# Kernel tuning notes

Measured on AMD Instinct MI355X. Metric: run time of the kernel, lower is better.

## Reference

```python
import jax, jax.numpy as jnp
import numpy as np

USER_NUM = 100000
ITEM_NUM = 50000
EMBED_DIM = 64
N_LAYERS = 2
NNZ_UU, NNZ_UI, NNZ_II = 1600000, 2000000, 800000


def setup_inputs() -> dict:
    key = jax.random.key(0)
    ks = jax.random.split(key, 11)
    return {
        "user_embedding": jax.random.normal(ks[0], (USER_NUM, EMBED_DIM), jnp.float32),
        "item_embedding": jax.random.normal(ks[1], (ITEM_NUM, EMBED_DIM), jnp.float32),
        "uu_val": jax.random.uniform(ks[2], (NNZ_UU,), jnp.float32),
        "ui_val": jax.random.uniform(ks[3], (NNZ_UI,), jnp.float32),
        "ii_val": jax.random.uniform(ks[4], (NNZ_II,), jnp.float32),
        "uu_rows": jax.random.randint(ks[5], (NNZ_UU,), 0, USER_NUM, jnp.int32),
        "uu_cols": jax.random.randint(ks[6], (NNZ_UU,), 0, USER_NUM, jnp.int32),
        "ui_rows": jax.random.randint(ks[7], (NNZ_UI,), 0, USER_NUM, jnp.int32),
        "ui_cols": jax.random.randint(ks[8], (NNZ_UI,), 0, ITEM_NUM, jnp.int32),
        "ii_rows": jax.random.randint(ks[9], (NNZ_II,), 0, ITEM_NUM, jnp.int32),
        "ii_cols": jax.random.randint(ks[10], (NNZ_II,), 0, ITEM_NUM, jnp.int32),
    }


def _spmm(rows, cols, vals, x, n_out):
    # sparse(COO) @ dense: gather source features, scale by edge value, scatter-add to rows
    return jax.ops.segment_sum(vals[:, None] * x[cols], rows, num_segments=n_out)


def reference(user_embedding, item_embedding, uu_val, ui_val, ii_val,
              uu_rows, uu_cols, ui_rows, ui_cols, ii_rows, ii_cols):
    u = user_embedding
    i = item_embedding
    # running sum for mean over (n_layers + 1) layer outputs
    u_sum, i_sum = u, i
    for _ in range(N_LAYERS):
        u_from_i = _spmm(ui_rows, ui_cols, ui_val, i, USER_NUM)        # user_item_graph @ item
        i_from_u = _spmm(ui_cols, ui_rows, ui_val, u, ITEM_NUM)        # user_item_graph.T @ user
        uu = _spmm(uu_rows, uu_cols, uu_val, u, USER_NUM)              # user_graph @ user
        ii = _spmm(ii_rows, ii_cols, ii_val, i, ITEM_NUM)              # item_graph @ item
        u = 0.5 * (uu + u_from_i)   # mean over stacked pair
        i = 0.5 * (ii + i_from_u)
        u_sum = u_sum + u
        i_sum = i_sum + i
    inv = 1.0 / (N_LAYERS + 1)
    return u_sum * inv, i_sum * inv
```

## Files before the change

### kernel.cpp

```cpp
#include <hip/hip_runtime.h>

typedef _Float16 half8_t __attribute__((ext_vector_type(8)));
typedef _Float16 half4_t __attribute__((ext_vector_type(4)));

#define NU 100000
#define NI 50000
#define NR (NU + NI)
#define D 64
#define COARSE 1024
#define RPB 147
#define CAP 8800
#define CHUNK 6144
#define RPT 6
#define NT4 (NR * 16)

__global__ void init_kernel(const float4* __restrict__ ue, const float4* __restrict__ ie,
                            float4* __restrict__ out, half4_t* __restrict__ curh) {
    int idx = blockIdx.x * 256 + threadIdx.x;
    if (idx >= NT4) return;
    float4 v = (idx < NU * 16) ? ue[idx] : ie[idx - NU * 16];
    out[idx] = v;
    half4_t h;
    h[0] = (_Float16)v.x; h[1] = (_Float16)v.y; h[2] = (_Float16)v.z; h[3] = (_Float16)v.w;
    curh[idx] = h;
}

__device__ __forceinline__ int place_dest(int p, const int* ui_r, const int* ui_c,
                                          const int* uu_r, const int* ii_r,
                                          int n_ui, int n_uu) {
    if (p < 2 * n_ui) {
        int e = p >> 1;
        return (p & 1) ? NU + ui_c[e] : ui_r[e];
    } else if (p < 2 * n_ui + n_uu) {
        return uu_r[p - 2 * n_ui];
    } else {
        return NU + ii_r[p - 2 * n_ui - n_uu];
    }
}

__global__ void count_kernel(const int* __restrict__ ui_r, const int* __restrict__ ui_c,
                             const int* __restrict__ uu_r, const int* __restrict__ ii_r,
                             int* __restrict__ m, int n_ui, int n_uu, int nnzt) {
    __shared__ int cnt[COARSE];
    int tid = threadIdx.x;
    cnt[tid] = 0;
    __syncthreads();
    int blk0 = blockIdx.x * CHUNK;
#pragma unroll
    for (int k = 0; k < RPT; k++) {
        int p = blk0 + k * 1024 + tid;
        if (p < nnzt) {
            int dest = place_dest(p, ui_r, ui_c, uu_r, ii_r, n_ui, n_uu);
            atomicAdd(&cnt[dest / RPB], 1);
        }
    }
    __syncthreads();
    m[blockIdx.x * COARSE + tid] = cnt[tid];
}

__global__ void colsum_kernel(const int* __restrict__ m, int* __restrict__ tots, int nblk) {
    __shared__ int s[256];
    int c = blockIdx.x, tid = threadIdx.x;
    int sum = 0;
    for (int b = tid; b < nblk; b += 256) sum += m[b * COARSE + c];
    s[tid] = sum;
    __syncthreads();
    for (int off = 128; off > 0; off >>= 1) {
        if (tid < off) s[tid] += s[tid + off];
        __syncthreads();
    }
    if (tid == 0) tots[c] = s[0];
}

__global__ void scan1_kernel(const int* __restrict__ tots, int* __restrict__ coarse_base,
                             int* __restrict__ ptr_nr) {
    __shared__ int s[COARSE];
    int tid = threadIdx.x;
    int x = tots[tid];
    s[tid] = x;
    __syncthreads();
    for (int off = 1; off < COARSE; off <<= 1) {
        int t = (tid >= off) ? s[tid - off] : 0;
        __syncthreads();
        s[tid] += t;
        __syncthreads();
    }
    coarse_base[tid] = s[tid] - x;
    if (tid == COARSE - 1) {
        coarse_base[COARSE] = s[tid];
        *ptr_nr = s[tid];
    }
}

__global__ void rebase_kernel(int* __restrict__ m, const int* __restrict__ coarse_base, int nblk) {
    __shared__ int s[256];
    int c = blockIdx.x, tid = threadIdx.x;
    int K = (nblk + 255) / 256;
    int b0 = tid * K;
    int b1 = b0 + K;
    if (b1 > nblk) b1 = nblk;
    int sum = 0;
    for (int b = b0; b < b1; b++) sum += m[b * COARSE + c];
    s[tid] = sum;
    __syncthreads();
    for (int off = 1; off < 256; off <<= 1) {
        int t = (tid >= off) ? s[tid - off] : 0;
        __syncthreads();
        s[tid] += t;
        __syncthreads();
    }
    int run = coarse_base[c] + s[tid] - sum;
    for (int b = b0; b < b1; b++) {
        int v = m[b * COARSE + c];
        m[b * COARSE + c] = run;
        run += v;
    }
}

__global__ void place_kernel(const int* __restrict__ ui_r, const int* __restrict__ ui_c,
                             const float* __restrict__ ui_v,
                             const int* __restrict__ uu_r, const int* __restrict__ uu_c,
                             const float* __restrict__ uu_v,
                             const int* __restrict__ ii_r, const int* __restrict__ ii_c,
                             const float* __restrict__ ii_v,
                             const int* __restrict__ m, uint2* __restrict__ scratch,
                             int n_ui, int n_uu, int nnzt) {
    __shared__ uint2 rec[CHUNK];
    __shared__ int cnt[COARSE];
    __shared__ int lbase[COARSE];
    __shared__ int base_s[COARSE];
    __shared__ int s_ntot;
    int tid = threadIdx.x;
    cnt[tid] = 0;
    __syncthreads();
    int blk0 = blockIdx.x * CHUNK;
    int rk[RPT];
#pragma unroll
    for (int k = 0; k < RPT; k++) {
        int p = blk0 + k * 1024 + tid;
        rk[k] = -1;
        if (p < nnzt) {
            int dest = place_dest(p, ui_r, ui_c, uu_r, ii_r, n_ui, n_uu);
            int c = dest / RPB;
            int lr = atomicAdd(&cnt[c], 1);
            rk[k] = (c << 14) | lr;
        }
    }
    __syncthreads();
    int own = cnt[tid];
    lbase[tid] = own;
    __syncthreads();
    for (int off = 1; off < COARSE; off <<= 1) {
        int t = (tid >= off) ? lbase[tid - off] : 0;
        __syncthreads();
        lbase[tid] += t;
        __syncthreads();
    }
    int incl = lbase[tid];
    __syncthreads();
    lbase[tid] = incl - own;
    if (tid == COARSE - 1) s_ntot = incl;
    base_s[tid] = m[blockIdx.x * COARSE + tid];
    __syncthreads();
#pragma unroll
    for (int k = 0; k < RPT; k++) {
        int p = blk0 + k * 1024 + tid;
        if (p >= nnzt) continue;
        int dest, src;
        float v;
        if (p < 2 * n_ui) {
            int e = p >> 1;
            int r = ui_r[e], cc = ui_c[e];
            v = ui_v[e];
            if (p & 1) { dest = NU + cc; src = r; }
            else       { dest = r; src = NU + cc; }
        } else if (p < 2 * n_ui + n_uu) {
            int e = p - 2 * n_ui;
            dest = uu_r[e]; src = uu_c[e]; v = uu_v[e];
        } else {
            int e = p - 2 * n_ui - n_uu;
            dest = NU + ii_r[e]; src = NU + ii_c[e]; v = ii_v[e];
        }
        int c  = rk[k] >> 14;
        int lr = rk[k] & 0x3FFF;
        int dl = dest - c * RPB;
        _Float16 hv = (_Float16)v;
        unsigned short us;
        __builtin_memcpy(&us, &hv, 2);
        rec[lbase[c] + lr] = make_uint2(((unsigned)dl << 18) | (unsigned)src,
                                        ((unsigned)c << 16) | (unsigned)us);
    }
    __syncthreads();
    int ntot = s_ntot;
    for (int i = tid; i < ntot; i += 1024) {
        uint2 r = rec[i];
        int c = r.y >> 16;
        scratch[base_s[c] + (i - lbase[c])] = r;
    }
}

__global__ void csr_kernel(const uint2* __restrict__ scratch, const int* __restrict__ coarse_base,
                           int* __restrict__ ptr, int* __restrict__ pk_src,
                           unsigned short* __restrict__ pk_val) {
    __shared__ int s[1024];
    __shared__ int fine[256];
    __shared__ int fill[256];
    __shared__ int lsrc[CAP];
    __shared__ unsigned short lval[CAP];
    int c = blockIdx.x, tid = threadIdx.x;
    int rbeg = c * RPB;
    int rcnt = NR - rbeg;
    if (rcnt > RPB) rcnt = RPB;
    if (rcnt < 0) rcnt = 0;
    int base = coarse_base[c], end = coarse_base[c + 1];
    int n = end - base;
    if (tid < 256) fine[tid] = 0;
    __syncthreads();
    for (int i = tid; i < n; i += 1024)
        atomicAdd(&fine[scratch[base + i].x >> 18], 1);
    __syncthreads();
    int own = (tid < 256) ? fine[tid] : 0;
    s[tid] = own;
    __syncthreads();
    for (int off = 1; off < 256; off <<= 1) {
        int t = (tid >= off) ? s[tid - off] : 0;
        __syncthreads();
        s[tid] += t;
        __syncthreads();
    }
    int excl = s[tid] - own;
    if (tid < rcnt) ptr[rbeg + tid] = base + excl;
    if (tid < 256) fill[tid] = excl;
    __syncthreads();
    if (n <= CAP) {
        for (int i = tid; i < n; i += 1024) {
            uint2 rec = scratch[base + i];
            int dl = rec.x >> 18;
            int slot = atomicAdd(&fill[dl], 1);
            lsrc[slot] = rec.x & 0x3FFFF;
            lval[slot] = (unsigned short)rec.y;
        }
        __syncthreads();
        for (int i = tid; i < n; i += 1024) {
            pk_src[base + i] = lsrc[i] << 7;
            pk_val[base + i] = lval[i];
        }
    } else {
        for (int i = tid; i < n; i += 1024) {
            uint2 rec = scratch[base + i];
            int dl = rec.x >> 18;
            int slot = atomicAdd(&fill[dl], 1);
            pk_src[base + slot] = (rec.x & 0x3FFFF) << 7;
            pk_val[base + slot] = (unsigned short)rec.y;
        }
    }
}

__global__ void spmm_fused(const int* __restrict__ ptr, const int* __restrict__ pk_src,
                           const _Float16* __restrict__ pk_val,
                           const half8_t* __restrict__ src,
                           half8_t* __restrict__ nexth, float4* __restrict__ out,
                           float final_scale, int store_next) {
    int w = (int)((blockIdx.x * blockDim.x + threadIdx.x) >> 6);
    int lane = threadIdx.x & 63;
    if (w >= NR) return;
    int g = lane >> 3;
    int fl = lane & 7;
    const char* sp = (const char*)src;
    int flo = fl * 16;

    int b = ptr[w], e = ptr[w + 1];
    float acc[8];
#pragma unroll
    for (int k = 0; k < 8; k++) acc[k] = 0.f;

    for (int j = b; j < e; j += 32) {
#pragma unroll
        for (int t = 0; t < 4; t++) {
            int jt = j + 8 * t + g;
            int it = (jt < e) ? jt : b;
            int st = pk_src[it];
            float vt = (jt < e) ? (float)pk_val[it] : 0.f;
            half8_t xt = *(const half8_t*)(sp + st + flo);
#pragma unroll
            for (int k = 0; k < 8; k++) acc[k] += vt * (float)xt[k];
        }
    }

#pragma unroll
    for (int k = 0; k < 8; k++) {
        acc[k] += __shfl_xor(acc[k], 8);
        acc[k] += __shfl_xor(acc[k], 16);
        acc[k] += __shfl_xor(acc[k], 32);
    }

    if (lane < 8) {
        float h[8];
#pragma unroll
        for (int k = 0; k < 8; k++) h[k] = 0.5f * acc[k];
        if (store_next) {
            half8_t hh;
#pragma unroll
            for (int k = 0; k < 8; k++) hh[k] = (_Float16)h[k];
            nexth[w * 8 + lane] = hh;
        }
        float4* op = out + (size_t)w * 16 + lane * 2;
        float4 o0 = op[0];
        float4 o1 = op[1];
        o0.x = (o0.x + h[0]) * final_scale;
        o0.y = (o0.y + h[1]) * final_scale;
        o0.z = (o0.z + h[2]) * final_scale;
        o0.w = (o0.w + h[3]) * final_scale;
        o1.x = (o1.x + h[4]) * final_scale;
        o1.y = (o1.y + h[5]) * final_scale;
        o1.z = (o1.z + h[6]) * final_scale;
        o1.w = (o1.w + h[7]) * final_scale;
        op[0] = o0;
        op[1] = o1;
    }
}

extern "C" void kernel_launch(void* const* d_in, const int* in_sizes, int n_in,
                              void* d_out, int out_size, void* d_ws, size_t ws_size,
                              hipStream_t stream) {
    const float* ue      = (const float*)d_in[0];
    const float* ie      = (const float*)d_in[1];
    const float* uu_val  = (const float*)d_in[2];
    const float* ui_val  = (const float*)d_in[3];
    const float* ii_val  = (const float*)d_in[4];
    const int*   uu_rows = (const int*)d_in[5];
    const int*   uu_cols = (const int*)d_in[6];
    const int*   ui_rows = (const int*)d_in[7];
    const int*   ui_cols = (const int*)d_in[8];
    const int*   ii_rows = (const int*)d_in[9];
    const int*   ii_cols = (const int*)d_in[10];

    const int NNZ_UU = in_sizes[2];
    const int NNZ_UI = in_sizes[3];
    const int NNZ_II = in_sizes[4];
    const int NNZT   = 2 * NNZ_UI + NNZ_UU + NNZ_II;
    const int NBLK   = (NNZT + CHUNK - 1) / CHUNK;

    float* out = (float*)d_out;

    char* wsb = (char*)d_ws;
    half8_t* curh   = (half8_t*)wsb;
    uint2*   scratch = (uint2*)(wsb + (size_t)NR * 128);
    half8_t* nexth  = (half8_t*)scratch;
    int*     pk_src = (int*)(scratch + NNZT);
    unsigned short* pk_val = (unsigned short*)(pk_src + NNZT);
    int*     ptr    = (int*)(pk_val + NNZT);
    int*     coarse_base = ptr + (NR + 1);
    int*     tots   = coarse_base + (COARSE + 1);
    int*     m      = tots + COARSE;

    init_kernel<<<(NT4 + 255) / 256, 256, 0, stream>>>(
        (const float4*)ue, (const float4*)ie, (float4*)out, (half4_t*)curh);

    count_kernel<<<NBLK, 1024, 0, stream>>>(
        ui_rows, ui_cols, uu_rows, ii_rows, m, NNZ_UI, NNZ_UU, NNZT);

    colsum_kernel<<<COARSE, 256, 0, stream>>>(m, tots, NBLK);
    scan1_kernel<<<1, 1024, 0, stream>>>(tots, coarse_base, ptr + NR);
    rebase_kernel<<<COARSE, 256, 0, stream>>>(m, coarse_base, NBLK);

    place_kernel<<<NBLK, 1024, 0, stream>>>(
        ui_rows, ui_cols, ui_val, uu_rows, uu_cols, uu_val,
        ii_rows, ii_cols, ii_val, m, scratch, NNZ_UI, NNZ_UU, NNZT);

    csr_kernel<<<COARSE, 1024, 0, stream>>>(scratch, coarse_base, ptr, pk_src, pk_val);

    int blocks = (NR * 64 + 511) / 512;

    spmm_fused<<<blocks, 512, 0, stream>>>(
        ptr, pk_src, (const _Float16*)pk_val, curh, nexth, (float4*)out, 1.0f, 1);

    spmm_fused<<<blocks, 512, 0, stream>>>(
        ptr, pk_src, (const _Float16*)pk_val, nexth, curh, (float4*)out, 1.0f / 3.0f, 0);
}
```

Measured before the change: 515.4 us.

## Pad CSR rows to multiples of four for vectorized edge loads in SpMM

The CSR build now pads each row's edge list to a multiple of four, with zero-filled slots and per-coarse-block slack, so row pointers are 4-aligned. The SpMM kernel then reads source indices as int4 and values as half4, each lane group handling eight edges per iteration with eight independent gathers in flight. This is meant to cut the number of index/value load instructions and raise memory-level parallelism in the gather loop. In exchange the padded edge arrays are larger, padded slots still gather row 0 with zero weight, and csr_kernel does extra zeroing work.

```diff
diff --git a/kernel.cpp b/kernel.cpp
--- a/kernel.cpp
+++ b/kernel.cpp
@@ -13,6 +13,7 @@
 #define CHUNK 6144
 #define RPT 6
 #define NT4 (NR * 16)
+#define PKSLACK 448
 
 __global__ void init_kernel(const float4* __restrict__ ue, const float4* __restrict__ ie,
                             float4* __restrict__ out, half4_t* __restrict__ curh) {
@@ -207,6 +208,7 @@
     __shared__ int fill[256];
     __shared__ int lsrc[CAP];
     __shared__ unsigned short lval[CAP];
+    __shared__ int s_pn;
     int c = blockIdx.x, tid = threadIdx.x;
     int rbeg = c * RPB;
     int rcnt = NR - rbeg;
@@ -214,13 +216,16 @@
     if (rcnt < 0) rcnt = 0;
     int base = coarse_base[c], end = coarse_base[c + 1];
     int n = end - base;
+    int pkc    = ((base + 3) & ~3) + c * PKSLACK;
+    int pknext = ((end  + 3) & ~3) + (c + 1) * PKSLACK;
     if (tid < 256) fine[tid] = 0;
     __syncthreads();
     for (int i = tid; i < n; i += 1024)
         atomicAdd(&fine[scratch[base + i].x >> 18], 1);
     __syncthreads();
     int own = (tid < 256) ? fine[tid] : 0;
-    s[tid] = own;
+    int own4 = (own + 3) & ~3;
+    s[tid] = own4;
     __syncthreads();
     for (int off = 1; off < 256; off <<= 1) {
         int t = (tid >= off) ? s[tid - off] : 0;
@@ -228,11 +233,16 @@
         s[tid] += t;
         __syncthreads();
     }
-    int excl = s[tid] - own;
-    if (tid < rcnt) ptr[rbeg + tid] = base + excl;
-    if (tid < 256) fill[tid] = excl;
-    __syncthreads();
-    if (n <= CAP) {
+    int excl4 = s[tid] - own4;
+    if (tid < rcnt) ptr[rbeg + tid] = pkc + excl4;
+    if (tid == 0 && rbeg + rcnt == NR) ptr[NR] = pknext;
+    if (tid < 256) fill[tid] = excl4;
+    if (tid == 255) s_pn = s[255];
+    __syncthreads();
+    int pn = s_pn;
+    if (pn <= CAP) {
+        for (int i = tid; i < pn; i += 1024) { lsrc[i] = 0; lval[i] = 0; }
+        __syncthreads();
         for (int i = tid; i < n; i += 1024) {
             uint2 rec = scratch[base + i];
             int dl = rec.x >> 18;
@@ -241,23 +251,26 @@
             lval[slot] = (unsigned short)rec.y;
         }
         __syncthreads();
-        for (int i = tid; i < n; i += 1024) {
-            pk_src[base + i] = lsrc[i] << 7;
-            pk_val[base + i] = lval[i];
-        }
+        for (int i = tid; i < pn; i += 1024) {
+            pk_src[pkc + i] = lsrc[i] << 7;
+            pk_val[pkc + i] = lval[i];
+        }
+        for (int i = pkc + pn + tid; i < pknext; i += 1024) { pk_src[i] = 0; pk_val[i] = 0; }
     } else {
+        for (int i = pkc + tid; i < pknext; i += 1024) { pk_src[i] = 0; pk_val[i] = 0; }
+        __syncthreads();
         for (int i = tid; i < n; i += 1024) {
             uint2 rec = scratch[base + i];
             int dl = rec.x >> 18;
             int slot = atomicAdd(&fill[dl], 1);
-            pk_src[base + slot] = (rec.x & 0x3FFFF) << 7;
-            pk_val[base + slot] = (unsigned short)rec.y;
+            pk_src[pkc + slot] = (rec.x & 0x3FFFF) << 7;
+            pk_val[pkc + slot] = (unsigned short)rec.y;
         }
     }
 }
 
 __global__ void spmm_fused(const int* __restrict__ ptr, const int* __restrict__ pk_src,
-                           const _Float16* __restrict__ pk_val,
+                           const half4_t* __restrict__ pk_val4,
                            const half8_t* __restrict__ src,
                            half8_t* __restrict__ nexth, float4* __restrict__ out,
                            float final_scale, int store_next) {
@@ -266,24 +279,45 @@
     if (w >= NR) return;
     int g = lane >> 3;
     int fl = lane & 7;
-    const char* sp = (const char*)src;
-    int flo = fl * 16;
+    const char* sph = (const char*)src + (fl << 4);
+    const int4* ps = (const int4*)pk_src;
 
     int b = ptr[w], e = ptr[w + 1];
+    int q0 = b >> 2, qe = e >> 2;
+
     float acc[8];
 #pragma unroll
     for (int k = 0; k < 8; k++) acc[k] = 0.f;
 
-    for (int j = b; j < e; j += 32) {
-#pragma unroll
-        for (int t = 0; t < 4; t++) {
-            int jt = j + 8 * t + g;
-            int it = (jt < e) ? jt : b;
-            int st = pk_src[it];
-            float vt = (jt < e) ? (float)pk_val[it] : 0.f;
-            half8_t xt = *(const half8_t*)(sp + st + flo);
-#pragma unroll
-            for (int k = 0; k < 8; k++) acc[k] += vt * (float)xt[k];
+    for (int q = q0 + g; q < qe; q += 16) {
+        int qb = q + 8;
+        int4 sa = ps[q];
+        half4_t va = pk_val4[q];
+        int4 sb = ps[qb];
+        half4_t vb = pk_val4[qb];
+        if (qb >= qe) {
+            sb = make_int4(0, 0, 0, 0);
+            half4_t z = {};
+            vb = z;
+        }
+        half8_t x0 = *(const half8_t*)(sph + sa.x);
+        half8_t x1 = *(const half8_t*)(sph + sa.y);
+        half8_t x2 = *(const half8_t*)(sph + sa.z);
+        half8_t x3 = *(const half8_t*)(sph + sa.w);
+        half8_t x4 = *(const half8_t*)(sph + sb.x);
+        half8_t x5 = *(const half8_t*)(sph + sb.y);
+        half8_t x6 = *(const half8_t*)(sph + sb.z);
+        half8_t x7 = *(const half8_t*)(sph + sb.w);
+#pragma unroll
+        for (int k = 0; k < 8; k++) {
+            acc[k] += (float)va[0] * (float)x0[k];
+            acc[k] += (float)va[1] * (float)x1[k];
+            acc[k] += (float)va[2] * (float)x2[k];
+            acc[k] += (float)va[3] * (float)x3[k];
+            acc[k] += (float)vb[0] * (float)x4[k];
+            acc[k] += (float)vb[1] * (float)x5[k];
+            acc[k] += (float)vb[2] * (float)x6[k];
+            acc[k] += (float)vb[3] * (float)x7[k];
         }
     }
 
@@ -340,6 +374,7 @@
     const int NNZ_II = in_sizes[4];
     const int NNZT   = 2 * NNZ_UI + NNZ_UU + NNZ_II;
     const int NBLK   = (NNZT + CHUNK - 1) / CHUNK;
+    const int PKTOT  = NNZT + PKSLACK * COARSE + 64;
 
     float* out = (float*)d_out;
 
@@ -348,8 +383,8 @@
     uint2*   scratch = (uint2*)(wsb + (size_t)NR * 128);
     half8_t* nexth  = (half8_t*)scratch;
     int*     pk_src = (int*)(scratch + NNZT);
-    unsigned short* pk_val = (unsigned short*)(pk_src + NNZT);
-    int*     ptr    = (int*)(pk_val + NNZT);
+    unsigned short* pk_val = (unsigned short*)(pk_src + PKTOT);
+    int*     ptr    = (int*)(pk_val + PKTOT);
     int*     coarse_base = ptr + (NR + 1);
     int*     tots   = coarse_base + (COARSE + 1);
     int*     m      = tots + COARSE;
@@ -373,8 +408,8 @@
     int blocks = (NR * 64 + 511) / 512;
 
     spmm_fused<<<blocks, 512, 0, stream>>>(
-        ptr, pk_src, (const _Float16*)pk_val, curh, nexth, (float4*)out, 1.0f, 1);
+        ptr, pk_src, (const half4_t*)pk_val, curh, nexth, (float4*)out, 1.0f, 1);
 
     spmm_fused<<<blocks, 512, 0, stream>>>(
-        ptr, pk_src, (const _Float16*)pk_val, nexth, curh, (float4*)out, 1.0f / 3.0f, 0);
-}
+        ptr, pk_src, (const half4_t*)pk_val, nexth, curh, (float4*)out, 1.0f / 3.0f, 0);
+}
```

Result: slower. 556.7 us (+8.0%).

## Segment CSR by source-column range and process four rows per 8-lane group

Applied to the files above, without the earlier changes.

The CSR build now buckets edges by source segment (src>>14) and by 1024-row destination chunk. This produces ten per-segment row-pointer arrays, so during SpMM all gathers within a segment pass touch a limited slice of the source features, which should improve L2 locality. The SpMM kernel is rewritten so each 8-lane group owns four consecutive rows, looping over segments with 4-way unrolled edge processing instead of one wavefront per row. In exchange it adds ten pointer reads per row, serial per-row loops that can load-imbalance on long rows, and heavier scans in the preprocessing.

```diff
diff --git a/kernel.cpp b/kernel.cpp
--- a/kernel.cpp
+++ b/kernel.cpp
@@ -7,8 +7,10 @@
 #define NI 50000
 #define NR (NU + NI)
 #define D 64
-#define COARSE 1024
-#define RPB 147
+#define SEG 10
+#define SEGSH 14
+#define CHK 147
+#define COARSE (SEG * CHK)
 #define CAP 8800
 #define CHUNK 6144
 #define RPT 6
@@ -25,37 +27,45 @@
     curh[idx] = h;
 }
 
-__device__ __forceinline__ int place_dest(int p, const int* ui_r, const int* ui_c,
-                                          const int* uu_r, const int* ii_r,
-                                          int n_ui, int n_uu) {
+__device__ __forceinline__ void place_ds(int p, const int* ui_r, const int* ui_c,
+                                         const int* uu_r, const int* uu_c,
+                                         const int* ii_r, const int* ii_c,
+                                         int n_ui, int n_uu, int& dest, int& src) {
     if (p < 2 * n_ui) {
         int e = p >> 1;
-        return (p & 1) ? NU + ui_c[e] : ui_r[e];
+        int r = ui_r[e], c = ui_c[e];
+        if (p & 1) { dest = NU + c; src = r; }
+        else       { dest = r;      src = NU + c; }
     } else if (p < 2 * n_ui + n_uu) {
-        return uu_r[p - 2 * n_ui];
+        int e = p - 2 * n_ui;
+        dest = uu_r[e]; src = uu_c[e];
     } else {
-        return NU + ii_r[p - 2 * n_ui - n_uu];
+        int e = p - 2 * n_ui - n_uu;
+        dest = NU + ii_r[e]; src = NU + ii_c[e];
     }
 }
 
 __global__ void count_kernel(const int* __restrict__ ui_r, const int* __restrict__ ui_c,
-                             const int* __restrict__ uu_r, const int* __restrict__ ii_r,
+                             const int* __restrict__ uu_r, const int* __restrict__ uu_c,
+                             const int* __restrict__ ii_r, const int* __restrict__ ii_c,
                              int* __restrict__ m, int n_ui, int n_uu, int nnzt) {
     __shared__ int cnt[COARSE];
     int tid = threadIdx.x;
-    cnt[tid] = 0;
+    for (int i = tid; i < COARSE; i += 1024) cnt[i] = 0;
     __syncthreads();
     int blk0 = blockIdx.x * CHUNK;
 #pragma unroll
     for (int k = 0; k < RPT; k++) {
         int p = blk0 + k * 1024 + tid;
         if (p < nnzt) {
-            int dest = place_dest(p, ui_r, ui_c, uu_r, ii_r, n_ui, n_uu);
-            atomicAdd(&cnt[dest / RPB], 1);
-        }
-    }
-    __syncthreads();
-    m[blockIdx.x * COARSE + tid] = cnt[tid];
+            int dest, src;
+            place_ds(p, ui_r, ui_c, uu_r, uu_c, ii_r, ii_c, n_ui, n_uu, dest, src);
+            int key = (src >> SEGSH) * CHK + (dest >> 10);
+            atomicAdd(&cnt[key], 1);
+        }
+    }
+    __syncthreads();
+    for (int i = tid; i < COARSE; i += 1024) m[blockIdx.x * COARSE + i] = cnt[i];
 }
 
 __global__ void colsum_kernel(const int* __restrict__ m, int* __restrict__ tots, int nblk) {
@@ -72,24 +82,23 @@
     if (tid == 0) tots[c] = s[0];
 }
 
-__global__ void scan1_kernel(const int* __restrict__ tots, int* __restrict__ coarse_base,
-                             int* __restrict__ ptr_nr) {
-    __shared__ int s[COARSE];
+__global__ void scan1_kernel(const int* __restrict__ tots, int* __restrict__ coarse_base) {
+    __shared__ int s[2048];
     int tid = threadIdx.x;
-    int x = tots[tid];
-    s[tid] = x;
-    __syncthreads();
-    for (int off = 1; off < COARSE; off <<= 1) {
-        int t = (tid >= off) ? s[tid - off] : 0;
-        __syncthreads();
-        s[tid] += t;
-        __syncthreads();
-    }
-    coarse_base[tid] = s[tid] - x;
-    if (tid == COARSE - 1) {
-        coarse_base[COARSE] = s[tid];
-        *ptr_nr = s[tid];
-    }
+    int x0 = (tid < COARSE) ? tots[tid] : 0;
+    int x1 = (tid + 1024 < COARSE) ? tots[tid + 1024] : 0;
+    s[tid] = x0; s[tid + 1024] = x1;
+    __syncthreads();
+    for (int off = 1; off < 2048; off <<= 1) {
+        int a = (tid >= off) ? s[tid - off] : 0;
+        int b = (tid + 1024 >= off) ? s[tid + 1024 - off] : 0;
+        __syncthreads();
+        s[tid] += a; s[tid + 1024] += b;
+        __syncthreads();
+    }
+    if (tid < COARSE) coarse_base[tid] = s[tid] - x0;
+    if (tid + 1024 < COARSE) coarse_base[tid + 1024] = s[tid + 1024] - x1;
+    if (tid == 0) coarse_base[COARSE] = s[2047];
 }
 
 __global__ void rebase_kernel(int* __restrict__ m, const int* __restrict__ coarse_base, int nblk) {
@@ -126,12 +135,11 @@
                              const int* __restrict__ m, uint2* __restrict__ scratch,
                              int n_ui, int n_uu, int nnzt) {
     __shared__ uint2 rec[CHUNK];
-    __shared__ int cnt[COARSE];
-    __shared__ int lbase[COARSE];
+    __shared__ int cnt[2048];
+    __shared__ int lb[2048];
     __shared__ int base_s[COARSE];
-    __shared__ int s_ntot;
     int tid = threadIdx.x;
-    cnt[tid] = 0;
+    cnt[tid] = 0; cnt[tid + 1024] = 0;
     __syncthreads();
     int blk0 = blockIdx.x * CHUNK;
     int rk[RPT];
@@ -140,27 +148,25 @@
         int p = blk0 + k * 1024 + tid;
         rk[k] = -1;
         if (p < nnzt) {
-            int dest = place_dest(p, ui_r, ui_c, uu_r, ii_r, n_ui, n_uu);
-            int c = dest / RPB;
-            int lr = atomicAdd(&cnt[c], 1);
-            rk[k] = (c << 14) | lr;
-        }
-    }
-    __syncthreads();
-    int own = cnt[tid];
-    lbase[tid] = own;
-    __syncthreads();
-    for (int off = 1; off < COARSE; off <<= 1) {
-        int t = (tid >= off) ? lbase[tid - off] : 0;
-        __syncthreads();
-        lbase[tid] += t;
-        __syncthreads();
-    }
-    int incl = lbase[tid];
-    __syncthreads();
-    lbase[tid] = incl - own;
-    if (tid == COARSE - 1) s_ntot = incl;
-    base_s[tid] = m[blockIdx.x * COARSE + tid];
+            int dest, src;
+            place_ds(p, ui_r, ui_c, uu_r, uu_c, ii_r, ii_c, n_ui, n_uu, dest, src);
+            int key = (src >> SEGSH) * CHK + (dest >> 10);
+            int lr = atomicAdd(&cnt[key], 1);
+            rk[k] = (key << 14) | lr;
+        }
+    }
+    __syncthreads();
+    int o0 = cnt[tid], o1 = cnt[tid + 1024];
+    lb[tid] = o0; lb[tid + 1024] = o1;
+    __syncthreads();
+    for (int off = 1; off < 2048; off <<= 1) {
+        int a = (tid >= off) ? lb[tid - off] : 0;
+        int b = (tid + 1024 >= off) ? lb[tid + 1024 - off] : 0;
+        __syncthreads();
+        lb[tid] += a; lb[tid + 1024] += b;
+        __syncthreads();
+    }
+    for (int i = tid; i < COARSE; i += 1024) base_s[i] = m[blockIdx.x * COARSE + i];
     __syncthreads();
 #pragma unroll
     for (int k = 0; k < RPT; k++) {
@@ -183,62 +189,64 @@
         }
         int c  = rk[k] >> 14;
         int lr = rk[k] & 0x3FFF;
-        int dl = dest - c * RPB;
+        int dl = dest & 1023;
         _Float16 hv = (_Float16)v;
         unsigned short us;
         __builtin_memcpy(&us, &hv, 2);
-        rec[lbase[c] + lr] = make_uint2(((unsigned)dl << 18) | (unsigned)src,
-                                        ((unsigned)c << 16) | (unsigned)us);
-    }
-    __syncthreads();
-    int ntot = s_ntot;
+        rec[(lb[c] - cnt[c]) + lr] = make_uint2(((unsigned)dl << 18) | (unsigned)src,
+                                                ((unsigned)c << 16) | (unsigned)us);
+    }
+    __syncthreads();
+    int ntot = lb[2047];
     for (int i = tid; i < ntot; i += 1024) {
         uint2 r = rec[i];
         int c = r.y >> 16;
-        scratch[base_s[c] + (i - lbase[c])] = r;
+        scratch[base_s[c] + (i - (lb[c] - cnt[c]))] = r;
     }
 }
 
 __global__ void csr_kernel(const uint2* __restrict__ scratch, const int* __restrict__ coarse_base,
-                           int* __restrict__ ptr, int* __restrict__ pk_src,
+                           int* __restrict__ P, int* __restrict__ pk_src,
                            unsigned short* __restrict__ pk_val) {
     __shared__ int s[1024];
-    __shared__ int fine[256];
-    __shared__ int fill[256];
+    __shared__ int fine[1024];
+    __shared__ int fill[1024];
     __shared__ int lsrc[CAP];
     __shared__ unsigned short lval[CAP];
     int c = blockIdx.x, tid = threadIdx.x;
-    int rbeg = c * RPB;
+    int seg = c / CHK, chunk = c % CHK;
+    int rbeg = chunk << 10;
     int rcnt = NR - rbeg;
-    if (rcnt > RPB) rcnt = RPB;
+    if (rcnt > 1024) rcnt = 1024;
     if (rcnt < 0) rcnt = 0;
     int base = coarse_base[c], end = coarse_base[c + 1];
     int n = end - base;
-    if (tid < 256) fine[tid] = 0;
+    fine[tid] = 0;
     __syncthreads();
     for (int i = tid; i < n; i += 1024)
         atomicAdd(&fine[scratch[base + i].x >> 18], 1);
     __syncthreads();
-    int own = (tid < 256) ? fine[tid] : 0;
+    int own = fine[tid];
     s[tid] = own;
     __syncthreads();
-    for (int off = 1; off < 256; off <<= 1) {
+    for (int off = 1; off < 1024; off <<= 1) {
         int t = (tid >= off) ? s[tid - off] : 0;
         __syncthreads();
         s[tid] += t;
         __syncthreads();
     }
     int excl = s[tid] - own;
-    if (tid < rcnt) ptr[rbeg + tid] = base + excl;
-    if (tid < 256) fill[tid] = excl;
+    if (tid < rcnt) P[seg * NR + rbeg + tid] = base + excl;
+    if (c == COARSE - 1 && tid == 0) P[SEG * NR] = coarse_base[COARSE];
+    fill[tid] = excl;
     __syncthreads();
     if (n <= CAP) {
         for (int i = tid; i < n; i += 1024) {
-            uint2 rec = scratch[base + i];
-            int dl = rec.x >> 18;
+            uint2 r = scratch[base + i];
+            int dl = r.x >> 18;
             int slot = atomicAdd(&fill[dl], 1);
-            lsrc[slot] = rec.x & 0x3FFFF;
-            lval[slot] = (unsigned short)rec.y;
+            lsrc[slot] = r.x & 0x3FFFF;
+            lval[slot] = (unsigned short)r.y;
         }
         __syncthreads();
         for (int i = tid; i < n; i += 1024) {
@@ -247,77 +255,96 @@
         }
     } else {
         for (int i = tid; i < n; i += 1024) {
-            uint2 rec = scratch[base + i];
-            int dl = rec.x >> 18;
+            uint2 r = scratch[base + i];
+            int dl = r.x >> 18;
             int slot = atomicAdd(&fill[dl], 1);
-            pk_src[base + slot] = (rec.x & 0x3FFFF) << 7;
-            pk_val[base + slot] = (unsigned short)rec.y;
-        }
-    }
-}
-
-__global__ void spmm_fused(const int* __restrict__ ptr, const int* __restrict__ pk_src,
-                           const _Float16* __restrict__ pk_val,
-                           const half8_t* __restrict__ src,
-                           half8_t* __restrict__ nexth, float4* __restrict__ out,
-                           float final_scale, int store_next) {
-    int w = (int)((blockIdx.x * blockDim.x + threadIdx.x) >> 6);
-    int lane = threadIdx.x & 63;
-    if (w >= NR) return;
-    int g = lane >> 3;
-    int fl = lane & 7;
-    const char* sp = (const char*)src;
-    int flo = fl * 16;
-
-    int b = ptr[w], e = ptr[w + 1];
-    float acc[8];
-#pragma unroll
-    for (int k = 0; k < 8; k++) acc[k] = 0.f;
-
-    for (int j = b; j < e; j += 32) {
-#pragma unroll
-        for (int t = 0; t < 4; t++) {
-            int jt = j + 8 * t + g;
-            int it = (jt < e) ? jt : b;
-            int st = pk_src[it];
-            float vt = (jt < e) ? (float)pk_val[it] : 0.f;
-            half8_t xt = *(const half8_t*)(sp + st + flo);
-#pragma unroll
-            for (int k = 0; k < 8; k++) acc[k] += vt * (float)xt[k];
-        }
-    }
-
-#pragma unroll
-    for (int k = 0; k < 8; k++) {
-        acc[k] += __shfl_xor(acc[k], 8);
-        acc[k] += __shfl_xor(acc[k], 16);
-        acc[k] += __shfl_xor(acc[k], 32);
-    }
-
-    if (lane < 8) {
-        float h[8];
-#pragma unroll
-        for (int k = 0; k < 8; k++) h[k] = 0.5f * acc[k];
-        if (store_next) {
-            half8_t hh;
-#pragma unroll
-            for (int k = 0; k < 8; k++) hh[k] = (_Float16)h[k];
-            nexth[w * 8 + lane] = hh;
-        }
-        float4* op = out + (size_t)w * 16 + lane * 2;
-        float4 o0 = op[0];
-        float4 o1 = op[1];
-        o0.x = (o0.x + h[0]) * final_scale;
-        o0.y = (o0.y + h[1]) * final_scale;
-        o0.z = (o0.z + h[2]) * final_scale;
-        o0.w = (o0.w + h[3]) * final_scale;
-        o1.x = (o1.x + h[4]) * final_scale;
-        o1.y = (o1.y + h[5]) * final_scale;
-        o1.z = (o1.z + h[6]) * final_scale;
-        o1.w = (o1.w + h[7]) * final_scale;
-        op[0] = o0;
-        op[1] = o1;
-    }
+            pk_src[base + slot] = (r.x & 0x3FFFF) << 7;
+            pk_val[base + slot] = (unsigned short)r.y;
+        }
+    }
+}
+
+__device__ __forceinline__ void run_row(int b, int e, const int* __restrict__ pk_src,
+                                        const _Float16* __restrict__ pk_val,
+                                        const char* __restrict__ sph, float (&acc)[8]) {
+    for (int j = b; j < e; j += 4) {
+        int j1 = (j + 1 < e) ? j + 1 : b;
+        int j2 = (j + 2 < e) ? j + 2 : b;
+        int j3 = (j + 3 < e) ? j + 3 : b;
+        int s0 = pk_src[j];
+        int s1 = pk_src[j1];
+        int s2 = pk_src[j2];
+        int s3 = pk_src[j3];
+        float v0 = (float)pk_val[j];
+        float v1 = (j + 1 < e) ? (float)pk_val[j1] : 0.f;
+        float v2 = (j + 2 < e) ? (float)pk_val[j2] : 0.f;
+        float v3 = (j + 3 < e) ? (float)pk_val[j3] : 0.f;
+        half8_t x0 = *(const half8_t*)(sph + s0);
+        half8_t x1 = *(const half8_t*)(sph + s1);
+        half8_t x2 = *(const half8_t*)(sph + s2);
+        half8_t x3 = *(const half8_t*)(sph + s3);
+#pragma unroll
+        for (int k = 0; k < 8; k++)
+            acc[k] += v0 * (float)x0[k] + v1 * (float)x1[k]
+                    + v2 * (float)x2[k] + v3 * (float)x3[k];
+    }
+}
+
+__device__ __forceinline__ void epi_row(int row, int fl, float (&a)[8],
+                                        half8_t* __restrict__ nexth, float4* __restrict__ out,
+                                        float final_scale, int store_next) {
+    float h[8];
+#pragma unroll
+    for (int k = 0; k < 8; k++) h[k] = 0.5f * a[k];
+    if (store_next) {
+        half8_t hh;
+#pragma unroll
+        for (int k = 0; k < 8; k++) hh[k] = (_Float16)h[k];
+        nexth[row * 8 + fl] = hh;
+    }
+    float4* op = out + (size_t)row * 16 + fl * 2;
+    float4 o0 = op[0];
+    float4 o1 = op[1];
+    o0.x = (o0.x + h[0]) * final_scale;
+    o0.y = (o0.y + h[1]) * final_scale;
+    o0.z = (o0.z + h[2]) * final_scale;
+    o0.w = (o0.w + h[3]) * final_scale;
+    o1.x = (o1.x + h[4]) * final_scale;
+    o1.y = (o1.y + h[5]) * final_scale;
+    o1.z = (o1.z + h[6]) * final_scale;
+    o1.w = (o1.w + h[7]) * final_scale;
+    op[0] = o0;
+    op[1] = o1;
+}
+
+__global__ void spmm_seg(const int* __restrict__ P, const int* __restrict__ pk_src,
+                         const _Float16* __restrict__ pk_val, const half8_t* __restrict__ src,
+                         half8_t* __restrict__ nexth, float4* __restrict__ out,
+                         float final_scale, int store_next) {
+    int gid = (int)((blockIdx.x * blockDim.x + threadIdx.x) >> 3);
+    int fl  = threadIdx.x & 7;
+    int r0  = gid << 2;
+    if (r0 >= NR) return;
+    const char* sph = (const char*)src + (fl << 4);
+
+    float a0[8], a1[8], a2[8], a3[8];
+#pragma unroll
+    for (int k = 0; k < 8; k++) { a0[k] = 0.f; a1[k] = 0.f; a2[k] = 0.f; a3[k] = 0.f; }
+
+    for (int sgi = 0; sgi < SEG; sgi++) {
+        const int* Ps = P + sgi * NR + r0;
+        int4 bb = *(const int4*)Ps;
+        int e3 = Ps[4];
+        run_row(bb.x, bb.y, pk_src, pk_val, sph, a0);
+        run_row(bb.y, bb.z, pk_src, pk_val, sph, a1);
+        run_row(bb.z, bb.w, pk_src, pk_val, sph, a2);
+        run_row(bb.w, e3,   pk_src, pk_val, sph, a3);
+    }
+
+    epi_row(r0 + 0, fl, a0, nexth, out, final_scale, store_next);
+    epi_row(r0 + 1, fl, a1, nexth, out, final_scale, store_next);
+    epi_row(r0 + 2, fl, a2, nexth, out, final_scale, store_next);
+    epi_row(r0 + 3, fl, a3, nexth, out, final_scale, store_next);
 }
 
 extern "C" void kernel_launch(void* const* d_in, const int* in_sizes, int n_in,
@@ -349,32 +376,38 @@
     half8_t* nexth  = (half8_t*)scratch;
     int*     pk_src = (int*)(scratch + NNZT);
     unsigned short* pk_val = (unsigned short*)(pk_src + NNZT);
-    int*     ptr    = (int*)(pk_val + NNZT);
-    int*     coarse_base = ptr + (NR + 1);
+    size_t moff = (size_t)NR * 128 + (size_t)NNZT * 14;
+    moff = (moff + 15) & ~(size_t)15;
+    int*     m = (int*)(wsb + moff);
+    int*     P = m;
+    size_t m_ints = (size_t)NBLK * COARSE;
+    size_t p_ints = (size_t)SEG * NR + 16;
+    if (m_ints < p_ints) m_ints = p_ints;
+    int*     coarse_base = m + m_ints;
     int*     tots   = coarse_base + (COARSE + 1);
-    int*     m      = tots + COARSE;
 
     init_kernel<<<(NT4 + 255) / 256, 256, 0, stream>>>(
         (const float4*)ue, (const float4*)ie, (float4*)out, (half4_t*)curh);
 
     count_kernel<<<NBLK, 1024, 0, stream>>>(
-        ui_rows, ui_cols, uu_rows, ii_rows, m, NNZ_UI, NNZ_UU, NNZT);
+        ui_rows, ui_cols, uu_rows, uu_cols, ii_rows, ii_cols, m, NNZ_UI, NNZ_UU, NNZT);
 
     colsum_kernel<<<COARSE, 256, 0, stream>>>(m, tots, NBLK);
-    scan1_kernel<<<1, 1024, 0, stream>>>(tots, coarse_base, ptr + NR);
+    scan1_kernel<<<1, 1024, 0, stream>>>(tots, coarse_base);
     rebase_kernel<<<COARSE, 256, 0, stream>>>(m, coarse_base, NBLK);
 
     place_kernel<<<NBLK, 1024, 0, stream>>>(
         ui_rows, ui_cols, ui_val, uu_rows, uu_cols, uu_val,
         ii_rows, ii_cols, ii_val, m, scratch, NNZ_UI, NNZ_UU, NNZT);
 
-    csr_kernel<<<COARSE, 1024, 0, stream>>>(scratch, coarse_base, ptr, pk_src, pk_val);
-
-    int blocks = (NR * 64 + 511) / 512;
-
-    spmm_fused<<<blocks, 512, 0, stream>>>(
-        ptr, pk_src, (const _Float16*)pk_val, curh, nexth, (float4*)out, 1.0f, 1);
-
-    spmm_fused<<<blocks, 512, 0, stream>>>(
-        ptr, pk_src, (const _Float16*)pk_val, nexth, curh, (float4*)out, 1.0f / 3.0f, 0);
-}
+    csr_kernel<<<COARSE, 1024, 0, stream>>>(scratch, coarse_base, P, pk_src, pk_val);
+
+    int groups = (NR + 3) / 4;
+    int sblocks = (groups + 31) / 32;
+
+    spmm_seg<<<sblocks, 256, 0, stream>>>(
+        P, pk_src, (const _Float16*)pk_val, curh, nexth, (float4*)out, 1.0f, 1);
+
+    spmm_seg<<<sblocks, 256, 0, stream>>>(
+        P, pk_src, (const _Float16*)pk_val, nexth, curh, (float4*)out, 1.0f / 3.0f, 0);
+}
```

Result: slower. 603.7 us (+17.1%).
